# Kernel tuning notes

Hardware: AMD Instinct MI355X
Metric: run time of the kernel (lower is better)

Reference implementation:

```python
import jax, jax.numpy as jnp
import numpy as np

OMEGA = 1.5

def _sine(x, W, b, omega=OMEGA):
    return jnp.sin(omega * (x @ W.T + b))

def setup_inputs() -> dict:
    key = jax.random.key(0)
    ks = jax.random.split(key, 17)
    I = J = K = 384
    mid, R = 256, 100
    s = 0.05  # small init scale, mimics uniform(-1/in, 1/in) style init
    return {
        "A_input": jax.random.normal(ks[0], (I, 1), jnp.float32),
        "B_input": jax.random.normal(ks[1], (J, 1), jnp.float32),
        "C_input": jax.random.normal(ks[2], (K, 1), jnp.float32),
        "A_W1": jax.random.normal(ks[3], (mid, 1), jnp.float32) * s,
        "A_b1": jax.random.normal(ks[4], (mid,), jnp.float32) * s,
        "A_W2": jax.random.normal(ks[5], (R, mid), jnp.float32) * s,
        "A_b2": jax.random.normal(ks[6], (R,), jnp.float32) * s,
        "B_W1": jax.random.normal(ks[7], (mid, 1), jnp.float32) * s,
        "B_b1": jax.random.normal(ks[8], (mid,), jnp.float32) * s,
        "B_W2": jax.random.normal(ks[9], (R, mid), jnp.float32) * s,
        "B_b2": jax.random.normal(ks[10], (R,), jnp.float32) * s,
        "C_W1": jax.random.normal(ks[11], (mid, 1), jnp.float32) * s,
        "C_b1": jax.random.normal(ks[12], (mid,), jnp.float32) * s,
        "C_W2": jax.random.normal(ks[13], (mid, mid), jnp.float32) * s,
        "C_b2": jax.random.normal(ks[14], (mid,), jnp.float32) * s,
        "C_W3": jax.random.normal(ks[15], (R, mid), jnp.float32) * s,
        "C_b3": jax.random.normal(ks[16], (R,), jnp.float32) * s,
    }

def reference(A_input, B_input, C_input,
              A_W1, A_b1, A_W2, A_b2,
              B_W1, B_b1, B_W2, B_b2,
              C_W1, C_b1, C_W2, C_b2, C_W3, C_b3):
    # Factor networks
    A = _sine(A_input, A_W1, A_b1) @ A_W2.T + A_b2                  # [I, R]
    B = _sine(B_input, B_W1, B_b1) @ B_W2.T + B_b2                  # [J, R]
    C = _sine(_sine(C_input, C_W1, C_b1), C_W2, C_b2) @ C_W3.T + C_b3  # [K, R]
    # The frozen core is super-diagonal (core[r,r,r]=1), so the permute/matmul
    # chain reduces exactly to the CP contraction sum_r A[i,r]*B[j,r]*C[k,r].
    return jnp.einsum('ir,jr,kr->ijk', A, B, C)  # [I, J, K]
```

## Files before the change

kernel.cpp:

```cpp
#include <hip/hip_runtime.h>
#include <hip/hip_bf16.h>

#define RR 100
#define MID 256
#define NN 384
#define KP 128

typedef __attribute__((ext_vector_type(8))) __bf16 bf16x8;
typedef __attribute__((ext_vector_type(4))) float floatx4;
typedef unsigned short ushort_t;

#define SW(row, ch) ((((row) << 7)) + ((((ch) ^ ((row) & 15))) << 3))

__device__ __forceinline__ ushort_t f2bf(float f) {
  __hip_bfloat16 h = __float2bfloat16(f);
  return __builtin_bit_cast(ushort_t, h);
}

__global__ __launch_bounds__(256) void factors_kernel(
    const float* __restrict__ xA, const float* __restrict__ xB,
    const float* __restrict__ xC,
    const float* __restrict__ AW1, const float* __restrict__ Ab1,
    const float* __restrict__ AW2, const float* __restrict__ Ab2,
    const float* __restrict__ BW1, const float* __restrict__ Bb1,
    const float* __restrict__ BW2, const float* __restrict__ Bb2,
    const float* __restrict__ CW1, const float* __restrict__ Cb1,
    const float* __restrict__ CW2, const float* __restrict__ Cb2,
    const float* __restrict__ CW3, const float* __restrict__ Cb3,
    float* __restrict__ Af, float* __restrict__ Bf,
    ushort_t* __restrict__ Cbf) {
  __shared__ float h[MID];
  __shared__ float h2[MID];
  const int i = blockIdx.x;
  const int net = blockIdx.y;
  const int t = threadIdx.x;

  const float* x  = (net == 0) ? xA  : (net == 1) ? xB  : xC;
  const float* W1 = (net == 0) ? AW1 : (net == 1) ? BW1 : CW1;
  const float* b1 = (net == 0) ? Ab1 : (net == 1) ? Bb1 : Cb1;

  const float xv = x[i];
  h[t] = sinf(1.5f * (xv * W1[t] + b1[t]));
  __syncthreads();

  const float* hlast = h;
  if (net == 2) {
    float acc = Cb2[t];
    const float* __restrict__ w = &CW2[t * MID];
#pragma unroll 4
    for (int m = 0; m < MID; m += 4) {
      const float4 wv = *(const float4*)&w[m];
      const float4 hv = *(const float4*)&h[m];
      acc += hv.x * wv.x;
      acc += hv.y * wv.y;
      acc += hv.z * wv.z;
      acc += hv.w * wv.w;
    }
    h2[t] = sinf(1.5f * acc);
    __syncthreads();
    hlast = h2;
  }

  const float* W2 = (net == 0) ? AW2 : (net == 1) ? BW2 : CW3;
  const float* b2 = (net == 0) ? Ab2 : (net == 1) ? Bb2 : Cb3;

  if (t < KP) {
    float v = 0.0f;
    if (t < RR) {
      float acc = b2[t];
      const float* __restrict__ w = &W2[t * MID];
#pragma unroll 4
      for (int m = 0; m < MID; m += 4) {
        const float4 wv = *(const float4*)&w[m];
        const float4 hv = *(const float4*)&hlast[m];
        acc += hv.x * wv.x;
        acc += hv.y * wv.y;
        acc += hv.z * wv.z;
        acc += hv.w * wv.w;
      }
      v = acc;
    }
    if (net == 0)      Af[i * KP + t] = v;
    else if (net == 1) Bf[i * KP + t] = v;
    else               Cbf[i * KP + t] = f2bf(v);
  }
}

__global__ __launch_bounds__(256, 3) void cp_mfma(
    const float* __restrict__ Af, const float* __restrict__ Bf,
    const ushort_t* __restrict__ Cbf, float* __restrict__ out) {
  __shared__ ushort_t Wt[64 * KP];
  __shared__ ushort_t Ct[128 * KP];

  const int i  = blockIdx.z;
  const int j0 = blockIdx.y * 64;
  const int k0 = blockIdx.x * 128;
  const int t  = threadIdx.x;

#pragma unroll
  for (int it = 0; it < 8; ++it) {
    const int idx = t + 256 * it;
    const int row = idx >> 4;
    const int ch  = idx & 15;
    *(uint4*)&Ct[SW(row, ch)] =
        *(const uint4*)&Cbf[(size_t)(k0 + row) * KP + ch * 8];
  }

  {
    const int jx = t >> 2;
    const int q  = t & 3;
    const float* __restrict__ arow = Af + (size_t)i * KP + q * 32;
    const float* __restrict__ brow = Bf + (size_t)(j0 + jx) * KP + q * 32;
#pragma unroll
    for (int c = 0; c < 4; ++c) {
      const float4 a0 = *(const float4*)(arow + c * 8);
      const float4 a1 = *(const float4*)(arow + c * 8 + 4);
      const float4 b0 = *(const float4*)(brow + c * 8);
      const float4 b1 = *(const float4*)(brow + c * 8 + 4);
      uint4 wv;
      wv.x = (unsigned)f2bf(a0.x * b0.x) | ((unsigned)f2bf(a0.y * b0.y) << 16);
      wv.y = (unsigned)f2bf(a0.z * b0.z) | ((unsigned)f2bf(a0.w * b0.w) << 16);
      wv.z = (unsigned)f2bf(a1.x * b1.x) | ((unsigned)f2bf(a1.y * b1.y) << 16);
      wv.w = (unsigned)f2bf(a1.z * b1.z) | ((unsigned)f2bf(a1.w * b1.w) << 16);
      *(uint4*)&Wt[SW(jx, q * 4 + c)] = wv;
    }
  }
  __syncthreads();

  const int lane = t & 63;
  const int w    = t >> 6;
  const int wj   = (w & 1) * 32;
  const int wk   = (w >> 1) * 64;
  const int m16  = lane & 15;
  const int g    = lane >> 4;

  floatx4 acc[4][2];
#pragma unroll
  for (int kf = 0; kf < 4; ++kf)
#pragma unroll
    for (int jf = 0; jf < 2; ++jf) acc[kf][jf] = (floatx4)0.0f;

#pragma unroll
  for (int ks = 0; ks < 4; ++ks) {
    bf16x8 cf[4], wfr[2];
#pragma unroll
    for (int kf = 0; kf < 4; ++kf)
      cf[kf] = *(const bf16x8*)&Ct[SW(wk + kf * 16 + m16, ks * 4 + g)];
#pragma unroll
    for (int jf = 0; jf < 2; ++jf)
      wfr[jf] = *(const bf16x8*)&Wt[SW(wj + jf * 16 + m16, ks * 4 + g)];
#pragma unroll
    for (int jf = 0; jf < 2; ++jf)
#pragma unroll
      for (int kf = 0; kf < 4; ++kf)
        acc[kf][jf] = __builtin_amdgcn_mfma_f32_16x16x32_bf16(
            cf[kf], wfr[jf], acc[kf][jf], 0, 0, 0);
  }

  const size_t ibase = (size_t)i * NN * NN;
#pragma unroll
  for (int kf = 0; kf < 4; ++kf) {
    const int k = k0 + wk + kf * 16 + g * 4;
#pragma unroll
    for (int jf = 0; jf < 2; ++jf) {
      const int j = j0 + wj + jf * 16 + m16;
      *(floatx4*)&out[ibase + (size_t)j * NN + k] = acc[kf][jf];
    }
  }
}

extern "C" void kernel_launch(void* const* d_in, const int* in_sizes, int n_in,
                              void* d_out, int out_size, void* d_ws, size_t ws_size,
                              hipStream_t stream) {
  const float* A_input = (const float*)d_in[0];
  const float* B_input = (const float*)d_in[1];
  const float* C_input = (const float*)d_in[2];
  const float* A_W1 = (const float*)d_in[3];
  const float* A_b1 = (const float*)d_in[4];
  const float* A_W2 = (const float*)d_in[5];
  const float* A_b2 = (const float*)d_in[6];
  const float* B_W1 = (const float*)d_in[7];
  const float* B_b1 = (const float*)d_in[8];
  const float* B_W2 = (const float*)d_in[9];
  const float* B_b2 = (const float*)d_in[10];
  const float* C_W1 = (const float*)d_in[11];
  const float* C_b1 = (const float*)d_in[12];
  const float* C_W2 = (const float*)d_in[13];
  const float* C_b2 = (const float*)d_in[14];
  const float* C_W3 = (const float*)d_in[15];
  const float* C_b3 = (const float*)d_in[16];

  float* Af = (float*)d_ws;
  float* Bf = Af + NN * KP;
  ushort_t* Cbf = (ushort_t*)(Bf + NN * KP);

  dim3 fgrid(NN, 3);
  factors_kernel<<<fgrid, 256, 0, stream>>>(
      A_input, B_input, C_input,
      A_W1, A_b1, A_W2, A_b2,
      B_W1, B_b1, B_W2, B_b2,
      C_W1, C_b1, C_W2, C_b2, C_W3, C_b3,
      Af, Bf, Cbf);

  dim3 grid(NN / 128, NN / 64, NN);
  cp_mfma<<<grid, 256, 0, stream>>>(Af, Bf, Cbf, (float*)d_out);
}
```

Before: 321.1 us.

## Loop over all k tiles per block and swizzle flattened block index

Each block now covers a full 64-row j slab for one i and loops over the three 128-wide k tiles, reusing the W=A*B product tile built once instead of rebuilding it per k tile. The grid is flattened to 1D with an XCD-style swizzle of the block index, and the warp layout changes to 16 j rows by 128 k columns per wave so each row writes contiguous 512-byte segments. The C tile is reloaded into LDS each iteration with extra barriers, which adds serialization within a block, and the grid shrinks threefold.

New measurement: 292.8 us. 1.1x faster.

```diff
diff --git a/kernel.cpp b/kernel.cpp
--- a/kernel.cpp
+++ b/kernel.cpp
@@ -92,19 +92,11 @@
   __shared__ ushort_t Wt[64 * KP];
   __shared__ ushort_t Ct[128 * KP];
 
-  const int i  = blockIdx.z;
-  const int j0 = blockIdx.y * 64;
-  const int k0 = blockIdx.x * 128;
-  const int t  = threadIdx.x;
-
-#pragma unroll
-  for (int it = 0; it < 8; ++it) {
-    const int idx = t + 256 * it;
-    const int row = idx >> 4;
-    const int ch  = idx & 15;
-    *(uint4*)&Ct[SW(row, ch)] =
-        *(const uint4*)&Cbf[(size_t)(k0 + row) * KP + ch * 8];
-  }
+  const int bid = blockIdx.x;
+  const int swz = (bid & 7) * 288 + (bid >> 3);
+  const int i   = swz / 6;
+  const int j0  = (swz % 6) * 64;
+  const int t   = threadIdx.x;
 
   {
     const int jx = t >> 2;
@@ -125,46 +117,47 @@
       *(uint4*)&Wt[SW(jx, q * 4 + c)] = wv;
     }
   }
-  __syncthreads();
 
   const int lane = t & 63;
   const int w    = t >> 6;
-  const int wj   = (w & 1) * 32;
-  const int wk   = (w >> 1) * 64;
   const int m16  = lane & 15;
   const int g    = lane >> 4;
+  const int jrow = j0 + w * 16 + m16;
+  const size_t obase = (size_t)i * NN * NN + (size_t)jrow * NN;
 
-  floatx4 acc[4][2];
-#pragma unroll
-  for (int kf = 0; kf < 4; ++kf)
-#pragma unroll
-    for (int jf = 0; jf < 2; ++jf) acc[kf][jf] = (floatx4)0.0f;
+#pragma unroll 1
+  for (int kt = 0; kt < 3; ++kt) {
+    __syncthreads();
 
 #pragma unroll
-  for (int ks = 0; ks < 4; ++ks) {
-    bf16x8 cf[4], wfr[2];
+    for (int it = 0; it < 8; ++it) {
+      const int idx = t + 256 * it;
+      const int row = idx >> 4;
+      const int ch  = idx & 15;
+      *(uint4*)&Ct[SW(row, ch)] =
+          *(const uint4*)&Cbf[(size_t)(kt * 128 + row) * KP + ch * 8];
+    }
+    __syncthreads();
+
+    floatx4 acc[8];
 #pragma unroll
-    for (int kf = 0; kf < 4; ++kf)
-      cf[kf] = *(const bf16x8*)&Ct[SW(wk + kf * 16 + m16, ks * 4 + g)];
+    for (int kf = 0; kf < 8; ++kf) acc[kf] = (floatx4)0.0f;
+
 #pragma unroll
-    for (int jf = 0; jf < 2; ++jf)
-      wfr[jf] = *(const bf16x8*)&Wt[SW(wj + jf * 16 + m16, ks * 4 + g)];
+    for (int ks = 0; ks < 4; ++ks) {
+      const bf16x8 wfr = *(const bf16x8*)&Wt[SW(w * 16 + m16, ks * 4 + g)];
 #pragma unroll
-    for (int jf = 0; jf < 2; ++jf)
+      for (int kf = 0; kf < 8; ++kf) {
+        const bf16x8 cf = *(const bf16x8*)&Ct[SW(kf * 16 + m16, ks * 4 + g)];
+        acc[kf] = __builtin_amdgcn_mfma_f32_16x16x32_bf16(
+            cf, wfr, acc[kf], 0, 0, 0);
+      }
+    }
+
+    const int kb = kt * 128 + g * 4;
 #pragma unroll
-      for (int kf = 0; kf < 4; ++kf)
-        acc[kf][jf] = __builtin_amdgcn_mfma_f32_16x16x32_bf16(
-            cf[kf], wfr[jf], acc[kf][jf], 0, 0, 0);
-  }
-
-  const size_t ibase = (size_t)i * NN * NN;
-#pragma unroll
-  for (int kf = 0; kf < 4; ++kf) {
-    const int k = k0 + wk + kf * 16 + g * 4;
-#pragma unroll
-    for (int jf = 0; jf < 2; ++jf) {
-      const int j = j0 + wj + jf * 16 + m16;
-      *(floatx4*)&out[ibase + (size_t)j * NN + k] = acc[kf][jf];
+    for (int kf = 0; kf < 8; ++kf) {
+      *(floatx4*)&out[obase + kb + kf * 16] = acc[kf];
     }
   }
 }
@@ -202,6 +195,5 @@
       C_W1, C_b1, C_W2, C_b2, C_W3, C_b3,
       Af, Bf, Cbf);
 
-  dim3 grid(NN / 128, NN / 64, NN);
-  cp_mfma<<<grid, 256, 0, stream>>>(Af, Bf, Cbf, (float*)d_out);
+  cp_mfma<<<dim3((NN / 64) * NN), 256, 0, stream>>>(Af, Bf, Cbf, (float*)d_out);
 }
```
